# Optimization experiments

Measured on AMD Instinct MI355X. Metric: run time of the kernel, lower is better.

The kernel has to match this reference:

```python
import jax, jax.numpy as jnp
import numpy as np
import math

B, S, D, H = 2, 2048, 1024, 16
HD = D // H
KL_GAMMA = 0.1
EPS = 1e-10


def setup_inputs() -> dict:
    key = jax.random.key(0)
    ks = jax.random.split(key, 12)
    # positive inputs + positive weights keep scores > 0 so log(mean(scores)) is finite
    query = jax.random.uniform(ks[0], (B, S, D), dtype=jnp.float32)
    k_in = jax.random.uniform(ks[1], (B, S, D), dtype=jnp.float32)
    v_in = jax.random.uniform(ks[2], (B, S, D), dtype=jnp.float32)
    def w(k):
        return jax.random.uniform(k, (D, D), dtype=jnp.float32) * 0.002
    b = jnp.full((D,), 1e-3, dtype=jnp.float32)
    return {
        "query": query, "key": k_in, "value": v_in,
        "Wq": w(ks[3]), "bq": b,
        "Wk": w(ks[4]), "bk": b,
        "Wv": w(ks[5]), "bv": b,
        "Wo": w(ks[6]), "bo": b,
    }


def reference(query, key, value, Wq, bq, Wk, bk, Wv, bv, Wo, bo):
    Bq, Sq, _ = query.shape
    Sk = key.shape[1]
    # projections, split heads: [B, H, S, HD]
    Q = (query @ Wq + bq).reshape(Bq, Sq, H, HD).transpose(0, 2, 1, 3)
    K = (key @ Wk + bk).reshape(Bq, Sk, H, HD).transpose(0, 2, 1, 3)
    V = (value @ Wv + bv).reshape(Bq, Sk, H, HD).transpose(0, 2, 1, 3)
    scores = jnp.einsum("bhqd,bhkd->bhqk", Q, K) / math.sqrt(HD)  # [B,H,Sq,Sk]
    # KL bias: row-mean broadcast over keys, then log
    target = jnp.mean(scores, axis=-1, keepdims=True)  # [B,H,Sq,1]
    scores = scores + KL_GAMMA * jnp.log(target + EPS)
    attn = jax.nn.softmax(scores, axis=-1)
    ctx = jnp.einsum("bhqk,bhkd->bhqd", attn, V)
    ctx = ctx.transpose(0, 2, 1, 3).reshape(Bq, Sq, D)
    return ctx @ Wo + bo
```

## Files before the change

kernel.cpp:

```cpp
#include <hip/hip_runtime.h>
#include <hip/hip_bf16.h>
#include <stdint.h>


#define NB 2
#define NS 2048
#define ND 1024
#define NH 16
#define HD 64

typedef short bf16x8 __attribute__((ext_vector_type(8)));
typedef short bf16x4 __attribute__((ext_vector_type(4)));
typedef float f32x4 __attribute__((ext_vector_type(4)));
typedef float f32x16 __attribute__((ext_vector_type(16)));
typedef unsigned int u32x4 __attribute__((ext_vector_type(4)));

static __device__ __forceinline__ short f2bf(float f) {
    uint32_t u = __builtin_bit_cast(uint32_t, f);
    uint32_t r = (u + 0x7fffu + ((u >> 16) & 1u)) >> 16;
    return (short)(uint16_t)r;
}

static __device__ __forceinline__ unsigned int cvtpk(float lo, float hi) {
    unsigned int r;
    asm("v_cvt_pk_bf16_f32 %0, %1, %2" : "=v"(r) : "v"(lo), "v"(hi));
    return r;
}

#if __has_builtin(__builtin_amdgcn_exp2f)
#define EXP2(x) __builtin_amdgcn_exp2f(x)
#else
#define EXP2(x) exp2f(x)
#endif

static __device__ __forceinline__ void plswap(unsigned& a, unsigned& b) {
#if __has_builtin(__builtin_amdgcn_permlane32_swap)
    auto r = __builtin_amdgcn_permlane32_swap(a, b, false, false);
    a = r[0]; b = r[1];
#else
    const int l = (int)(threadIdx.x & 63);
    unsigned bl = __shfl(b, l & 31);
    unsigned ah = __shfl(a, (l & 31) + 32);
    a = (l < 32) ? a : bl;
    b = (l < 32) ? ah : b;
#endif
}

typedef __attribute__((address_space(1))) const unsigned int glob_u32;
typedef __attribute__((address_space(3))) unsigned int lds_u32;
static __device__ __forceinline__ void gload16(const void* g, void* l) {
    __builtin_amdgcn_global_load_lds((glob_u32*)g, (lds_u32*)l, 16, 0, 0);
}

#define VMW(N) do { asm volatile("s_waitcnt vmcnt(" #N ")" ::: "memory"); \
                    __builtin_amdgcn_sched_barrier(0); } while (0)
#define BAR()  do { __builtin_amdgcn_s_barrier();                          \
                    __builtin_amdgcn_sched_barrier(0); } while (0)

__global__ __launch_bounds__(256) void prep_cast(const float* __restrict__ q,
                                                 const float* __restrict__ k,
                                                 const float* __restrict__ v,
                                                 short* __restrict__ Qo,
                                                 short* __restrict__ Ko,
                                                 short* __restrict__ Vo) {
    const float* src = (blockIdx.z == 0) ? q : (blockIdx.z == 1) ? k : v;
    short* dst = (blockIdx.z == 0) ? Qo : (blockIdx.z == 1) ? Ko : Vo;
    const size_t i = ((size_t)blockIdx.x * 256 + threadIdx.x) * 8;
    f32x4 a = *(const f32x4*)(src + i);
    f32x4 b = *(const f32x4*)(src + i + 4);
    bf16x8 o;
    o[0] = f2bf(a[0]); o[1] = f2bf(a[1]); o[2] = f2bf(a[2]); o[3] = f2bf(a[3]);
    o[4] = f2bf(b[0]); o[5] = f2bf(b[1]); o[6] = f2bf(b[2]); o[7] = f2bf(b[3]);
    *(bf16x8*)(dst + i) = o;
}

__global__ __launch_bounds__(256) void prep_wt(const float* __restrict__ W0,
                                               const float* __restrict__ W1,
                                               const float* __restrict__ W2,
                                               const float* __restrict__ W3,
                                               short* __restrict__ WtAll) {
    __shared__ short tile[32][33];
    const float* W = (blockIdx.z == 0) ? W0 : (blockIdx.z == 1) ? W1
                   : (blockIdx.z == 2) ? W2 : W3;
    short* Wt = WtAll + (size_t)blockIdx.z * (ND * ND);
    const int tx = threadIdx.x & 31;
    const int ty = threadIdx.x >> 5;
    const int k0 = blockIdx.x * 32, n0 = blockIdx.y * 32;
#pragma unroll
    for (int i = 0; i < 4; i++)
        tile[ty + i * 8][tx] = f2bf(W[(size_t)(k0 + ty + i * 8) * ND + n0 + tx]);
    __syncthreads();
#pragma unroll
    for (int i = 0; i < 4; i++)
        Wt[(size_t)(n0 + ty + i * 8) * ND + k0 + tx] = tile[tx][ty + i * 8];
}

static __device__ __forceinline__ void gemm_stage(const char* A, const char* W,
                                                  char* As3, char* Bs3,
                                                  int buf, int tile,
                                                  int gm, int gn, int lin) {
#pragma unroll
    for (int j = 0; j < 2; j++) {
        const int lj = lin + (j << 10);
        const int row = lj >> 6;
        const int colL = (lj & 63) ^ (((row ^ (row >> 2)) & 3) << 4);
        gload16(A + (size_t)(gm + row) * (ND * 2) + tile * 64 + colL,
                As3 + buf * 8192 + lj);
        gload16(W + (size_t)(gn + row) * (ND * 2) + tile * 64 + colL,
                Bs3 + buf * 8192 + lj);
    }
}

static __device__ __forceinline__ void gemm_step(const char* AsB, const char* BsB,
                                                 int wr, int wc, int r, int g,
                                                 f32x4 (&acc)[4][4]) {
    bf16x8 af[4], bfv[4];
#pragma unroll
    for (int m = 0; m < 4; m++) {
        const int ar = wr * 64 + m * 16 + r;
        const int fa = ((ar ^ (ar >> 2)) & 3) << 4;
        af[m] = *(const bf16x8*)(AsB + ar * 64 + ((g << 4) ^ fa));
    }
#pragma unroll
    for (int n = 0; n < 4; n++) {
        const int br = wc * 64 + n * 16 + r;
        const int fb = ((br ^ (br >> 2)) & 3) << 4;
        bfv[n] = *(const bf16x8*)(BsB + br * 64 + ((g << 4) ^ fb));
    }
#pragma unroll
    for (int m = 0; m < 4; m++)
#pragma unroll
        for (int n = 0; n < 4; n++)
            acc[m][n] = __builtin_amdgcn_mfma_f32_16x16x32_bf16(
                af[m], bfv[n], acc[m][n], 0, 0, 0);
}

static __device__ __forceinline__ void gemm_body(const short* __restrict__ A,
                                                 const short* __restrict__ Wt,
                                                 const float* __restrict__ bias,
                                                 void* __restrict__ Out,
                                                 int mode, float scale,
                                                 char* As3, char* Bs3) {
    const int tid = threadIdx.x;
    const int gm = blockIdx.x * 128;
    const int gn = blockIdx.y * 128;
    const int w = tid >> 6;
    const int l = tid & 63;
    const int r = l & 15;
    const int g = l >> 4;
    const int wr = w >> 1, wc = w & 1;
    const char* Ap = (const char*)A;
    const char* Wp = (const char*)Wt;

    f32x4 acc[4][4];
#pragma unroll
    for (int m = 0; m < 4; m++)
#pragma unroll
        for (int n = 0; n < 4; n++) acc[m][n] = (f32x4){0.f, 0.f, 0.f, 0.f};

    const int lin = ((w * 2) << 10) + l * 16;

    gemm_stage(Ap, Wp, As3, Bs3, 0, 0, gm, gn, lin);
    gemm_stage(Ap, Wp, As3, Bs3, 1, 1, gm, gn, lin);

    int cur = 0, stg = 2;
    for (int t = 0; t < ND / 32 - 2; t++) {
        gemm_stage(Ap, Wp, As3, Bs3, stg, t + 2, gm, gn, lin);
        VMW(8);
        BAR();
        gemm_step(As3 + cur * 8192, Bs3 + cur * 8192, wr, wc, r, g, acc);
        BAR();
        cur = (cur == 2) ? 0 : cur + 1;
        stg = (stg == 2) ? 0 : stg + 1;
    }
    VMW(4);
    BAR();
    gemm_step(As3 + cur * 8192, Bs3 + cur * 8192, wr, wc, r, g, acc);
    BAR();
    cur = (cur == 2) ? 0 : cur + 1;
    VMW(0);
    BAR();
    gemm_step(As3 + cur * 8192, Bs3 + cur * 8192, wr, wc, r, g, acc);

#pragma unroll
    for (int m = 0; m < 4; m++) {
        const int orow = gm + wr * 64 + m * 16 + g * 4;
#pragma unroll
        for (int n = 0; n < 4; n++) {
            const int ocol = gn + wc * 64 + n * 16 + r;
            const float bv = bias[ocol];
#pragma unroll
            for (int i = 0; i < 4; i++) {
                const float vout = (acc[m][n][i] + bv) * scale;
                const int row = orow + i;
                if (mode == 0) {
                    const int b = row >> 11, s = row & 2047;
                    const int h = ocol >> 6, hd = ocol & 63;
                    ((short*)Out)[(((size_t)(b * NH + h) * NS + s) << 6) + hd] = f2bf(vout);
                } else if (mode == 1) {
                    const int b = row >> 11, s = row & 2047;
                    const int h = ocol >> 6, hd = ocol & 63;
                    ((short*)Out)[((size_t)(b * NH + h) * HD + hd) * NS + s] = f2bf(vout);
                } else {
                    ((float*)Out)[(size_t)row * ND + ocol] = vout;
                }
            }
        }
    }
}

#define QSCALE 0.18033688011112042f

__global__ __launch_bounds__(256, 3) void gemm_qkv(const short* __restrict__ Qin,
                                                   const short* __restrict__ Kin,
                                                   const short* __restrict__ Vin,
                                                   const short* __restrict__ WtAll,
                                                   const float* __restrict__ bq,
                                                   const float* __restrict__ bk,
                                                   const float* __restrict__ bv,
                                                   short* __restrict__ Qo,
                                                   short* __restrict__ Ko,
                                                   short* __restrict__ Vto) {
    __shared__ __align__(16) char As[3 * 8192];
    __shared__ __align__(16) char Bs[3 * 8192];
    const int z = blockIdx.z;
    const short* A = (z == 0) ? Qin : (z == 1) ? Kin : Vin;
    const short* Wt = WtAll + (size_t)z * ND * ND;
    const float* bias = (z == 0) ? bq : (z == 1) ? bk : bv;
    void* Out = (z == 0) ? (void*)Qo : (z == 1) ? (void*)Ko : (void*)Vto;
    const float scale = (z == 0) ? QSCALE : 1.0f;
    const int mode = (z == 2) ? 1 : 0;
    gemm_body(A, Wt, bias, Out, mode, scale, As, Bs);
}

__global__ __launch_bounds__(256, 3) void gemm_fin(const short* __restrict__ Ctx,
                                                   const short* __restrict__ Wt,
                                                   const float* __restrict__ bo,
                                                   float* __restrict__ Out) {
    __shared__ __align__(16) char As[3 * 8192];
    __shared__ __align__(16) char Bs[3 * 8192];
    gemm_body(Ctx, Wt, bo, Out, 2, 1.0f, As, Bs);
}

static __device__ __forceinline__ void stage2(const char* Kp8, const char* Vp8,
                                              char* Kbuf, char* Vbuf,
                                              int t, int w, int l) {
#pragma unroll
    for (int jj = 0; jj < 2; jj++) {
        const int chunk = w * 2 + jj;
        const int half = chunk >> 3;
        const int lin = ((chunk & 7) << 10) + l * 16;
        const int sw = lin ^ (((lin >> 7) & 7) << 4);
        const int row = sw >> 7, col = sw & 127;
        gload16(Kp8 + (size_t)(half * 1024 + t * 64 + row) * 128 + col,
                Kbuf + half * 8192 + ((chunk & 7) << 10));
        gload16(Vp8 + (size_t)row * (NS * 2) + (half * 1024 + t * 64) * 2 + col,
                Vbuf + half * 8192 + ((chunk & 7) << 10));
    }
}

__global__ __launch_bounds__(512, 2) void attn_kern(const short* __restrict__ Q,
                                                    const short* __restrict__ K,
                                                    const short* __restrict__ Vt,
                                                    short* __restrict__ Ctx) {
    __shared__ __align__(16) char smem[2][2][16384];
    __shared__ float rsbuf[8][2][32];

    const int tid = threadIdx.x;
    const int w = tid >> 6;
    const int l = tid & 63;
    const int c = l & 31;
    const int h = l >> 5;
    const int h16 = h << 4;

    const int bid = blockIdx.x;
    const int swb = (bid & 7) * 32 + (bid >> 3);
    const int bh = swb >> 3;
    const int qt = swb & 7;
    const int g = w & 3;
    const int khalf = w >> 2;
    const int qw = qt * 256 + g * 64;

    const short* Qp = Q + (size_t)bh * NS * HD;
    const char* Kp8 = (const char*)(K + (size_t)bh * NS * HD);
    const char* Vp8 = (const char*)(Vt + (size_t)bh * HD * NS);

    bf16x8 qf[2][4];
#pragma unroll
    for (int qc = 0; qc < 2; qc++)
#pragma unroll
        for (int st = 0; st < 4; st++)
            qf[qc][st] = *(const bf16x8*)(Qp + (size_t)(qw + qc * 32 + c) * HD +
                                          st * 16 + h * 8);

    f32x16 acc[2][2];
#pragma unroll
    for (int qc = 0; qc < 2; qc++)
#pragma unroll
        for (int dt = 0; dt < 2; dt++) acc[qc][dt] = (f32x16)(0.f);
    float rs0 = 0.f, rs1 = 0.f;

    const int sx = (c & 7) << 4;

    stage2(Kp8, Vp8, smem[0][0], smem[0][1], 0, w, l);

    int bufi = 0;
#pragma unroll 1
    for (int t = 0; t < 16; t++) {
        if (t < 15) {
            stage2(Kp8, Vp8, smem[bufi ^ 1][0], smem[bufi ^ 1][1], t + 1, w, l);
            VMW(4);
        } else {
            VMW(0);
        }
        BAR();

        const char* Kt = smem[bufi][0] + khalf * 8192;
        const char* Vv = smem[bufi][1] + khalf * 8192;

#pragma unroll
        for (int ktile = 0; ktile < 2; ktile++) {
            bf16x8 kf[4];
#pragma unroll
            for (int st = 0; st < 4; st++)
                kf[st] = *(const bf16x8*)(Kt + ((ktile * 32 + c) << 7) +
                                          ((st * 32 + h16) ^ sx));
            f32x16 S0 = (f32x16)(0.f), S1 = (f32x16)(0.f);
#pragma unroll
            for (int st = 0; st < 4; st++) {
                S0 = __builtin_amdgcn_mfma_f32_32x32x16_bf16(kf[st], qf[0][st], S0, 0, 0, 0);
                S1 = __builtin_amdgcn_mfma_f32_32x32x16_bf16(kf[st], qf[1][st], S1, 0, 0, 0);
            }

            float tv0[16], tv1[16];
#pragma unroll
            for (int i = 0; i < 16; i++) {
                tv0[i] = EXP2(S0[i]); rs0 += tv0[i];
                tv1[i] = EXP2(S1[i]); rs1 += tv1[i];
            }
            unsigned p0a[4], p0b[4], p1a[4], p1b[4];
#pragma unroll
            for (int q4 = 0; q4 < 4; q4++) {
                p0a[q4] = cvtpk(tv0[4 * q4], tv0[4 * q4 + 1]);
                p0b[q4] = cvtpk(tv0[4 * q4 + 2], tv0[4 * q4 + 3]);
                p1a[q4] = cvtpk(tv1[4 * q4], tv1[4 * q4 + 1]);
                p1b[q4] = cvtpk(tv1[4 * q4 + 2], tv1[4 * q4 + 3]);
            }

#pragma unroll
            for (int ks = 0; ks < 2; ks++) {
                unsigned a0 = p0a[2 * ks], b0 = p0a[2 * ks + 1];
                unsigned a1 = p0b[2 * ks], b1 = p0b[2 * ks + 1];
                plswap(a0, b0); plswap(a1, b1);
                u32x4 pw0; pw0[0] = a0; pw0[1] = a1; pw0[2] = b0; pw0[3] = b1;
                bf16x8 pa0 = __builtin_bit_cast(bf16x8, pw0);
                unsigned c0 = p1a[2 * ks], d0 = p1a[2 * ks + 1];
                unsigned c1 = p1b[2 * ks], d1 = p1b[2 * ks + 1];
                plswap(c0, d0); plswap(c1, d1);
                u32x4 pw1; pw1[0] = c0; pw1[1] = c1; pw1[2] = d0; pw1[3] = d1;
                bf16x8 pa1 = __builtin_bit_cast(bf16x8, pw1);
#pragma unroll
                for (int dt = 0; dt < 2; dt++) {
                    bf16x8 vb = *(const bf16x8*)(Vv + ((dt * 32 + c) << 7) +
                                                 ((ktile * 64 + ks * 32 + h16) ^ sx));
                    acc[0][dt] = __builtin_amdgcn_mfma_f32_32x32x16_bf16(pa0, vb, acc[0][dt], 0, 0, 0);
                    acc[1][dt] = __builtin_amdgcn_mfma_f32_32x32x16_bf16(pa1, vb, acc[1][dt], 0, 0, 0);
                }
            }
        }
        BAR();
        bufi ^= 1;
    }

    rs0 += __shfl_xor(rs0, 32);
    rs1 += __shfl_xor(rs1, 32);
    if (h == 0) { rsbuf[w][0][c] = rs0; rsbuf[w][1][c] = rs1; }

    float* sumbuf = (float*)&smem[0][0][0];
    if (w >= 4) {
#pragma unroll
        for (int qc = 0; qc < 2; qc++)
#pragma unroll
            for (int q4 = 0; q4 < 4; q4++)
#pragma unroll
                for (int i = 0; i < 4; i++) {
                    const int qrow = qc * 32 + i + 8 * q4 + 4 * h;
#pragma unroll
                    for (int dt = 0; dt < 2; dt++)
                        sumbuf[((g * 64 + qrow) << 6) + dt * 32 + c] =
                            acc[qc][dt][q4 * 4 + i];
                }
    }
    __syncthreads();
    if (w < 4) {
        const int b = bh >> 4, hh = bh & 15;
#pragma unroll
        for (int qc = 0; qc < 2; qc++)
#pragma unroll
            for (int q4 = 0; q4 < 4; q4++)
#pragma unroll
                for (int i = 0; i < 4; i++) {
                    const int qrow32 = i + 8 * q4 + 4 * h;
                    const int qrow = qc * 32 + qrow32;
                    const float inv = 1.0f / (rsbuf[g][qc][qrow32] +
                                              rsbuf[4 + g][qc][qrow32]);
                    short* op = Ctx + ((size_t)b * NS + qt * 256 + g * 64 + qrow) * ND +
                                hh * HD;
#pragma unroll
                    for (int dt = 0; dt < 2; dt++) {
                        const float val = acc[qc][dt][q4 * 4 + i] +
                                          sumbuf[((g * 64 + qrow) << 6) + dt * 32 + c];
                        op[dt * 32 + c] = f2bf(val * inv);
                    }
                }
    }
}

extern "C" void kernel_launch(void* const* d_in, const int* in_sizes, int n_in,
                              void* d_out, int out_size, void* d_ws, size_t ws_size,
                              hipStream_t stream) {
    (void)in_sizes; (void)n_in; (void)out_size; (void)ws_size;
    const float* query = (const float*)d_in[0];
    const float* key_  = (const float*)d_in[1];
    const float* value = (const float*)d_in[2];
    const float* Wq = (const float*)d_in[3];
    const float* bq = (const float*)d_in[4];
    const float* Wk = (const float*)d_in[5];
    const float* bk = (const float*)d_in[6];
    const float* Wv = (const float*)d_in[7];
    const float* bv = (const float*)d_in[8];
    const float* Wo = (const float*)d_in[9];
    const float* bo = (const float*)d_in[10];

    char* ws = (char*)d_ws;
    const size_t MB = 1024 * 1024;
    short* WtAll = (short*)ws;
    short* Qin = (short*)(ws + 8 * MB);
    short* Kin = (short*)(ws + 16 * MB);
    short* Vin = (short*)(ws + 24 * MB);
    short* Qb  = (short*)(ws + 32 * MB);
    short* Kb  = (short*)(ws + 40 * MB);
    short* Vtb = (short*)(ws + 48 * MB);
    short* Ctx = (short*)(ws + 8 * MB);

    prep_cast<<<dim3(2048, 1, 3), 256, 0, stream>>>(query, key_, value, Qin, Kin, Vin);
    prep_wt<<<dim3(32, 32, 4), 256, 0, stream>>>(Wq, Wk, Wv, Wo, WtAll);
    gemm_qkv<<<dim3(32, 8, 3), 256, 0, stream>>>(Qin, Kin, Vin, WtAll, bq, bk, bv,
                                                 Qb, Kb, Vtb);
    attn_kern<<<dim3(256), 512, 0, stream>>>(Qb, Kb, Vtb, Ctx);
    gemm_fin<<<dim3(32, 8), 256, 0, stream>>>(Ctx, WtAll + 3 * ND * ND, bo, (float*)d_out);
}
```

Baseline: 118.2 us.

## Merge prep kernels and stream attention K/V directly into registers

Folds the input cast and weight-transpose kernels into a single launch, with each transpose block handling two tiles. The attention kernel no longer stages K and V tiles through shared memory with barriers. Instead it loads K and V fragments straight from global memory into two register buffers that alternate, and raises wave priority around the MFMA compute. It also adds scheduling fences in the GEMM stage and disables unrolling of the GEMM main loop. The aim is to cut a kernel launch and the LDS round-trips and barriers in attention, at the cost of uncoalesced global loads and higher register pressure.

Measured after the change: 144.6 us. +22.4%, slower.

```diff
diff --git a/kernel.cpp b/kernel.cpp
--- a/kernel.cpp
+++ b/kernel.cpp
@@ -56,44 +56,56 @@
                     __builtin_amdgcn_sched_barrier(0); } while (0)
 #define BAR()  do { __builtin_amdgcn_s_barrier();                          \
                     __builtin_amdgcn_sched_barrier(0); } while (0)
-
-__global__ __launch_bounds__(256) void prep_cast(const float* __restrict__ q,
-                                                 const float* __restrict__ k,
-                                                 const float* __restrict__ v,
-                                                 short* __restrict__ Qo,
-                                                 short* __restrict__ Ko,
-                                                 short* __restrict__ Vo) {
-    const float* src = (blockIdx.z == 0) ? q : (blockIdx.z == 1) ? k : v;
-    short* dst = (blockIdx.z == 0) ? Qo : (blockIdx.z == 1) ? Ko : Vo;
-    const size_t i = ((size_t)blockIdx.x * 256 + threadIdx.x) * 8;
-    f32x4 a = *(const f32x4*)(src + i);
-    f32x4 b = *(const f32x4*)(src + i + 4);
-    bf16x8 o;
-    o[0] = f2bf(a[0]); o[1] = f2bf(a[1]); o[2] = f2bf(a[2]); o[3] = f2bf(a[3]);
-    o[4] = f2bf(b[0]); o[5] = f2bf(b[1]); o[6] = f2bf(b[2]); o[7] = f2bf(b[3]);
-    *(bf16x8*)(dst + i) = o;
-}
-
-__global__ __launch_bounds__(256) void prep_wt(const float* __restrict__ W0,
-                                               const float* __restrict__ W1,
-                                               const float* __restrict__ W2,
-                                               const float* __restrict__ W3,
-                                               short* __restrict__ WtAll) {
+#define SFENCE() __builtin_amdgcn_sched_barrier(0)
+
+__global__ __launch_bounds__(256) void prep_all(const float* __restrict__ q,
+                                                const float* __restrict__ k,
+                                                const float* __restrict__ v,
+                                                const float* __restrict__ W0,
+                                                const float* __restrict__ W1,
+                                                const float* __restrict__ W2,
+                                                const float* __restrict__ W3,
+                                                short* __restrict__ Qo,
+                                                short* __restrict__ Ko,
+                                                short* __restrict__ Vo,
+                                                short* __restrict__ WtAll) {
     __shared__ short tile[32][33];
-    const float* W = (blockIdx.z == 0) ? W0 : (blockIdx.z == 1) ? W1
-                   : (blockIdx.z == 2) ? W2 : W3;
-    short* Wt = WtAll + (size_t)blockIdx.z * (ND * ND);
+    const int z = blockIdx.z;
+    if (z < 3) {
+        const float* src = (z == 0) ? q : (z == 1) ? k : v;
+        short* dst = (z == 0) ? Qo : (z == 1) ? Ko : Vo;
+        const size_t i = ((size_t)blockIdx.x * 256 + threadIdx.x) * 8;
+        f32x4 a = *(const f32x4*)(src + i);
+        f32x4 b = *(const f32x4*)(src + i + 4);
+        bf16x8 o;
+        o[0] = f2bf(a[0]); o[1] = f2bf(a[1]); o[2] = f2bf(a[2]); o[3] = f2bf(a[3]);
+        o[4] = f2bf(b[0]); o[5] = f2bf(b[1]); o[6] = f2bf(b[2]); o[7] = f2bf(b[3]);
+        *(bf16x8*)(dst + i) = o;
+        return;
+    }
     const int tx = threadIdx.x & 31;
     const int ty = threadIdx.x >> 5;
-    const int k0 = blockIdx.x * 32, n0 = blockIdx.y * 32;
-#pragma unroll
-    for (int i = 0; i < 4; i++)
-        tile[ty + i * 8][tx] = f2bf(W[(size_t)(k0 + ty + i * 8) * ND + n0 + tx]);
-    __syncthreads();
-#pragma unroll
-    for (int i = 0; i < 4; i++)
-        Wt[(size_t)(n0 + ty + i * 8) * ND + k0 + tx] = tile[tx][ty + i * 8];
-}
+#pragma unroll 1
+    for (int it = 0; it < 2; ++it) {
+        const int tt = blockIdx.x * 2 + it;
+        const int which = tt >> 10;
+        const float* W = (which == 0) ? W0 : (which == 1) ? W1
+                       : (which == 2) ? W2 : W3;
+        short* Wt = WtAll + (size_t)which * (ND * ND);
+        const int t = tt & 1023;
+        const int k0 = (t >> 5) * 32, n0 = (t & 31) * 32;
+#pragma unroll
+        for (int i = 0; i < 4; i++)
+            tile[ty + i * 8][tx] = f2bf(W[(size_t)(k0 + ty + i * 8) * ND + n0 + tx]);
+        __syncthreads();
+#pragma unroll
+        for (int i = 0; i < 4; i++)
+            Wt[(size_t)(n0 + ty + i * 8) * ND + k0 + tx] = tile[tx][ty + i * 8];
+        __syncthreads();
+    }
+}
+
+#define QSCALE 0.18033688011112042f
 
 static __device__ __forceinline__ void gemm_stage(const char* A, const char* W,
                                                   char* As3, char* Bs3,
@@ -109,6 +121,7 @@
         gload16(W + (size_t)(gn + row) * (ND * 2) + tile * 64 + colL,
                 Bs3 + buf * 8192 + lj);
     }
+    SFENCE();
 }
 
 static __device__ __forceinline__ void gemm_step(const char* AsB, const char* BsB,
@@ -164,6 +177,7 @@
     gemm_stage(Ap, Wp, As3, Bs3, 1, 1, gm, gn, lin);
 
     int cur = 0, stg = 2;
+#pragma unroll 1
     for (int t = 0; t < ND / 32 - 2; t++) {
         gemm_stage(Ap, Wp, As3, Bs3, stg, t + 2, gm, gn, lin);
         VMW(8);
@@ -208,8 +222,6 @@
         }
     }
 }
-
-#define QSCALE 0.18033688011112042f
 
 __global__ __launch_bounds__(256, 3) void gemm_qkv(const short* __restrict__ Qin,
                                                    const short* __restrict__ Kin,
@@ -234,36 +246,66 @@
 }
 
 __global__ __launch_bounds__(256, 3) void gemm_fin(const short* __restrict__ Ctx,
-                                                   const short* __restrict__ Wt,
+                                                   const short* __restrict__ WtAll,
                                                    const float* __restrict__ bo,
                                                    float* __restrict__ Out) {
     __shared__ __align__(16) char As[3 * 8192];
     __shared__ __align__(16) char Bs[3 * 8192];
-    gemm_body(Ctx, Wt, bo, Out, 2, 1.0f, As, Bs);
-}
-
-static __device__ __forceinline__ void stage2(const char* Kp8, const char* Vp8,
-                                              char* Kbuf, char* Vbuf,
-                                              int t, int w, int l) {
-#pragma unroll
-    for (int jj = 0; jj < 2; jj++) {
-        const int chunk = w * 2 + jj;
-        const int half = chunk >> 3;
-        const int lin = ((chunk & 7) << 10) + l * 16;
-        const int sw = lin ^ (((lin >> 7) & 7) << 4);
-        const int row = sw >> 7, col = sw & 127;
-        gload16(Kp8 + (size_t)(half * 1024 + t * 64 + row) * 128 + col,
-                Kbuf + half * 8192 + ((chunk & 7) << 10));
-        gload16(Vp8 + (size_t)row * (NS * 2) + (half * 1024 + t * 64) * 2 + col,
-                Vbuf + half * 8192 + ((chunk & 7) << 10));
-    }
-}
+    gemm_body(Ctx, WtAll + (size_t)3 * ND * ND, bo, Out, 2, 1.0f, As, Bs);
+}
+
+#define LDKF(ktg, KF)                                                         \
+  { _Pragma("unroll") for (int st = 0; st < 4; st++)                          \
+      KF[st] = *(const bf16x8*)(Kb + (size_t)((ktg) + c) * 128 + st * 32 + h16); \
+    SFENCE(); }
+
+#define LDVF(ktg, VB)                                                         \
+  { _Pragma("unroll") for (int dt = 0; dt < 2; dt++)                          \
+      _Pragma("unroll") for (int ks = 0; ks < 2; ks++)                        \
+        VB[dt][ks] = *(const bf16x8*)(Vb + (size_t)(dt * 32 + c) * (NS * 2) + \
+                                      (ktg) * 2 + ks * 32 + h16);             \
+    SFENCE(); }
+
+#define ACOMP(KF, VB)                                                         \
+  { f32x16 S0 = (f32x16)(0.f), S1 = (f32x16)(0.f);                           \
+    _Pragma("unroll") for (int st = 0; st < 4; st++) {                        \
+      S0 = __builtin_amdgcn_mfma_f32_32x32x16_bf16(KF[st], qf[0][st], S0, 0, 0, 0); \
+      S1 = __builtin_amdgcn_mfma_f32_32x32x16_bf16(KF[st], qf[1][st], S1, 0, 0, 0); \
+    }                                                                         \
+    float tv0[16], tv1[16];                                                   \
+    _Pragma("unroll") for (int i = 0; i < 16; i++) {                          \
+      tv0[i] = EXP2(S0[i]); rs0 += tv0[i];                                    \
+      tv1[i] = EXP2(S1[i]); rs1 += tv1[i];                                    \
+    }                                                                         \
+    unsigned p0a[4], p0b[4], p1a[4], p1b[4];                                  \
+    _Pragma("unroll") for (int q4 = 0; q4 < 4; q4++) {                        \
+      p0a[q4] = cvtpk(tv0[4 * q4], tv0[4 * q4 + 1]);                          \
+      p0b[q4] = cvtpk(tv0[4 * q4 + 2], tv0[4 * q4 + 3]);                      \
+      p1a[q4] = cvtpk(tv1[4 * q4], tv1[4 * q4 + 1]);                          \
+      p1b[q4] = cvtpk(tv1[4 * q4 + 2], tv1[4 * q4 + 3]);                      \
+    }                                                                         \
+    _Pragma("unroll") for (int ks = 0; ks < 2; ks++) {                        \
+      unsigned a0 = p0a[2 * ks], b0 = p0a[2 * ks + 1];                        \
+      unsigned a1 = p0b[2 * ks], b1 = p0b[2 * ks + 1];                        \
+      plswap(a0, b0); plswap(a1, b1);                                         \
+      u32x4 pw0; pw0[0] = a0; pw0[1] = a1; pw0[2] = b0; pw0[3] = b1;          \
+      bf16x8 pa0 = __builtin_bit_cast(bf16x8, pw0);                           \
+      unsigned c0 = p1a[2 * ks], d0 = p1a[2 * ks + 1];                        \
+      unsigned c1 = p1b[2 * ks], d1 = p1b[2 * ks + 1];                        \
+      plswap(c0, d0); plswap(c1, d1);                                         \
+      u32x4 pw1; pw1[0] = c0; pw1[1] = c1; pw1[2] = d0; pw1[3] = d1;          \
+      bf16x8 pa1 = __builtin_bit_cast(bf16x8, pw1);                           \
+      _Pragma("unroll") for (int dt = 0; dt < 2; dt++) {                      \
+        acc[0][dt] = __builtin_amdgcn_mfma_f32_32x32x16_bf16(pa0, VB[dt][ks], acc[0][dt], 0, 0, 0); \
+        acc[1][dt] = __builtin_amdgcn_mfma_f32_32x32x16_bf16(pa1, VB[dt][ks], acc[1][dt], 0, 0, 0); \
+      }                                                                       \
+    } }
 
 __global__ __launch_bounds__(512, 2) void attn_kern(const short* __restrict__ Q,
                                                     const short* __restrict__ K,
                                                     const short* __restrict__ Vt,
                                                     short* __restrict__ Ctx) {
-    __shared__ __align__(16) char smem[2][2][16384];
+    __shared__ float sumbuf[4 * 64 * 64];
     __shared__ float rsbuf[8][2][32];
 
     const int tid = threadIdx.x;
@@ -282,8 +324,10 @@
     const int qw = qt * 256 + g * 64;
 
     const short* Qp = Q + (size_t)bh * NS * HD;
-    const char* Kp8 = (const char*)(K + (size_t)bh * NS * HD);
-    const char* Vp8 = (const char*)(Vt + (size_t)bh * HD * NS);
+    const char* Kb = (const char*)(K + (size_t)bh * NS * HD) +
+                     (size_t)(khalf * 1024) * 128;
+    const char* Vb = (const char*)(Vt + (size_t)bh * HD * NS) +
+                     (size_t)(khalf * 1024) * 2;
 
     bf16x8 qf[2][4];
 #pragma unroll
@@ -300,83 +344,27 @@
         for (int dt = 0; dt < 2; dt++) acc[qc][dt] = (f32x16)(0.f);
     float rs0 = 0.f, rs1 = 0.f;
 
-    const int sx = (c & 7) << 4;
-
-    stage2(Kp8, Vp8, smem[0][0], smem[0][1], 0, w, l);
-
-    int bufi = 0;
+    bf16x8 kfA[4], kfB[4];
+    bf16x8 vbA[2][2], vbB[2][2];
+    LDKF(0, kfA); LDVF(0, vbA);
 #pragma unroll 1
-    for (int t = 0; t < 16; t++) {
-        if (t < 15) {
-            stage2(Kp8, Vp8, smem[bufi ^ 1][0], smem[bufi ^ 1][1], t + 1, w, l);
-            VMW(4);
-        } else {
-            VMW(0);
-        }
-        BAR();
-
-        const char* Kt = smem[bufi][0] + khalf * 8192;
-        const char* Vv = smem[bufi][1] + khalf * 8192;
-
-#pragma unroll
-        for (int ktile = 0; ktile < 2; ktile++) {
-            bf16x8 kf[4];
-#pragma unroll
-            for (int st = 0; st < 4; st++)
-                kf[st] = *(const bf16x8*)(Kt + ((ktile * 32 + c) << 7) +
-                                          ((st * 32 + h16) ^ sx));
-            f32x16 S0 = (f32x16)(0.f), S1 = (f32x16)(0.f);
-#pragma unroll
-            for (int st = 0; st < 4; st++) {
-                S0 = __builtin_amdgcn_mfma_f32_32x32x16_bf16(kf[st], qf[0][st], S0, 0, 0, 0);
-                S1 = __builtin_amdgcn_mfma_f32_32x32x16_bf16(kf[st], qf[1][st], S1, 0, 0, 0);
-            }
-
-            float tv0[16], tv1[16];
-#pragma unroll
-            for (int i = 0; i < 16; i++) {
-                tv0[i] = EXP2(S0[i]); rs0 += tv0[i];
-                tv1[i] = EXP2(S1[i]); rs1 += tv1[i];
-            }
-            unsigned p0a[4], p0b[4], p1a[4], p1b[4];
-#pragma unroll
-            for (int q4 = 0; q4 < 4; q4++) {
-                p0a[q4] = cvtpk(tv0[4 * q4], tv0[4 * q4 + 1]);
-                p0b[q4] = cvtpk(tv0[4 * q4 + 2], tv0[4 * q4 + 3]);
-                p1a[q4] = cvtpk(tv1[4 * q4], tv1[4 * q4 + 1]);
-                p1b[q4] = cvtpk(tv1[4 * q4 + 2], tv1[4 * q4 + 3]);
-            }
-
-#pragma unroll
-            for (int ks = 0; ks < 2; ks++) {
-                unsigned a0 = p0a[2 * ks], b0 = p0a[2 * ks + 1];
-                unsigned a1 = p0b[2 * ks], b1 = p0b[2 * ks + 1];
-                plswap(a0, b0); plswap(a1, b1);
-                u32x4 pw0; pw0[0] = a0; pw0[1] = a1; pw0[2] = b0; pw0[3] = b1;
-                bf16x8 pa0 = __builtin_bit_cast(bf16x8, pw0);
-                unsigned c0 = p1a[2 * ks], d0 = p1a[2 * ks + 1];
-                unsigned c1 = p1b[2 * ks], d1 = p1b[2 * ks + 1];
-                plswap(c0, d0); plswap(c1, d1);
-                u32x4 pw1; pw1[0] = c0; pw1[1] = c1; pw1[2] = d0; pw1[3] = d1;
-                bf16x8 pa1 = __builtin_bit_cast(bf16x8, pw1);
-#pragma unroll
-                for (int dt = 0; dt < 2; dt++) {
-                    bf16x8 vb = *(const bf16x8*)(Vv + ((dt * 32 + c) << 7) +
-                                                 ((ktile * 64 + ks * 32 + h16) ^ sx));
-                    acc[0][dt] = __builtin_amdgcn_mfma_f32_32x32x16_bf16(pa0, vb, acc[0][dt], 0, 0, 0);
-                    acc[1][dt] = __builtin_amdgcn_mfma_f32_32x32x16_bf16(pa1, vb, acc[1][dt], 0, 0, 0);
-                }
-            }
-        }
-        BAR();
-        bufi ^= 1;
+    for (int it = 0; it < 16; ++it) {
+        const int base = it * 64;
+        LDKF(base + 32, kfB); LDVF(base + 32, vbB);
+        __builtin_amdgcn_s_setprio(1);
+        ACOMP(kfA, vbA);
+        __builtin_amdgcn_s_setprio(0);
+        const int nxt = (it < 15) ? base + 64 : base + 32;
+        LDKF(nxt, kfA); LDVF(nxt, vbA);
+        __builtin_amdgcn_s_setprio(1);
+        ACOMP(kfB, vbB);
+        __builtin_amdgcn_s_setprio(0);
     }
 
     rs0 += __shfl_xor(rs0, 32);
     rs1 += __shfl_xor(rs1, 32);
     if (h == 0) { rsbuf[w][0][c] = rs0; rsbuf[w][1][c] = rs1; }
 
-    float* sumbuf = (float*)&smem[0][0][0];
     if (w >= 4) {
 #pragma unroll
         for (int qc = 0; qc < 2; qc++)
@@ -443,10 +431,11 @@
     short* Vtb = (short*)(ws + 48 * MB);
     short* Ctx = (short*)(ws + 8 * MB);
 
-    prep_cast<<<dim3(2048, 1, 3), 256, 0, stream>>>(query, key_, value, Qin, Kin, Vin);
-    prep_wt<<<dim3(32, 32, 4), 256, 0, stream>>>(Wq, Wk, Wv, Wo, WtAll);
-    gemm_qkv<<<dim3(32, 8, 3), 256, 0, stream>>>(Qin, Kin, Vin, WtAll, bq, bk, bv,
-                                                 Qb, Kb, Vtb);
+    prep_all<<<dim3(2048, 1, 4), 256, 0, stream>>>(query, key_, value,
+                                                   Wq, Wk, Wv, Wo,
+                                                   Qin, Kin, Vin, WtAll);
+    gemm_qkv<<<dim3(32, 8, 3), 256, 0, stream>>>(Qin, Kin, Vin, WtAll,
+                                                 bq, bk, bv, Qb, Kb, Vtb);
     attn_kern<<<dim3(256), 512, 0, stream>>>(Qb, Kb, Vtb, Ctx);
-    gemm_fin<<<dim3(32, 8), 256, 0, stream>>>(Ctx, WtAll + 3 * ND * ND, bo, (float*)d_out);
-}
+    gemm_fin<<<dim3(32, 8), 256, 0, stream>>>(Ctx, WtAll, bo, (float*)d_out);
+}
```
